# Optimization experiments

Hardware: AMD Instinct MI355X
Metric: run time of the kernel (lower is better)

The kernel has to match this reference:

```python
import jax, jax.numpy as jnp
import numpy as np

N = 100_000      # nodes
E = 1_600_000    # directed edges (before self-loops)
F_IN = 256       # input node features
H = 128          # hidden_dim
HEADS = 2
C_HEAD = H // HEADS  # 64, GATConv out_channels per head
G = 128          # graphs in batch
NCLS = 10
NEG_SLOPE = 0.2  # PyG GATConv default


def setup_inputs() -> dict:
    key = jax.random.key(0)
    ks = jax.random.split(key, 20)
    p = lambda k, shape: (jax.random.normal(k, shape, jnp.float32) * 0.05)
    x = jax.random.normal(ks[0], (N, F_IN), jnp.float32)
    edge_index = jax.random.randint(ks[1], (2, E), 0, N, dtype=jnp.int64)
    batch = jnp.sort(jax.random.randint(ks[2], (N,), 0, G, dtype=jnp.int64))
    return dict(
        x=x, edge_index=edge_index, batch=batch,
        pre_w=p(ks[3], (F_IN, H)), pre_b=p(ks[4], (H,)),
        w1=p(ks[5], (H, H)), asrc1=p(ks[6], (HEADS, C_HEAD)), adst1=p(ks[7], (HEADS, C_HEAD)), b1=p(ks[8], (H,)),
        w2=p(ks[9], (H, H)), asrc2=p(ks[10], (HEADS, C_HEAD)), adst2=p(ks[11], (HEADS, C_HEAD)), b2=p(ks[12], (H,)),
        post_w1=p(ks[13], (H, H)), post_b1=p(ks[14], (H,)),
        post_w2=p(ks[15], (H, NCLS)), post_b2=p(ks[16], (NCLS,)),
    )


def _gat_conv(h_in, w, a_src, a_dst, b, src, dst):
    # h: [N, heads, c]
    h = (h_in @ w).reshape(N, HEADS, C_HEAD)
    alpha_src = jnp.sum(h * a_src, axis=-1)  # [N, heads]
    alpha_dst = jnp.sum(h * a_dst, axis=-1)  # [N, heads]
    e = jax.nn.leaky_relu(alpha_src[src] + alpha_dst[dst], NEG_SLOPE)  # [E+N, heads]
    # numerically stable softmax over incoming edges of each destination node
    m = jax.ops.segment_max(e, dst, num_segments=N)
    ex = jnp.exp(e - m[dst])
    denom = jax.ops.segment_sum(ex, dst, num_segments=N)
    alpha = ex / denom[dst]                                           # [E+N, heads]
    out = jax.ops.segment_sum(h[src] * alpha[:, :, None], dst, num_segments=N)
    return out.reshape(N, H) + b  # concat heads + bias


def reference(x, edge_index, batch, pre_w, pre_b,
              w1, asrc1, adst1, b1, w2, asrc2, adst2, b2,
              post_w1, post_b1, post_w2, post_b2):
    # PyG GATConv default add_self_loops=True
    loop = jnp.arange(N, dtype=edge_index.dtype)
    src = jnp.concatenate([edge_index[0], loop])
    dst = jnp.concatenate([edge_index[1], loop])

    h = jax.nn.relu(x @ pre_w + pre_b)
    reprs = jax.ops.segment_sum(h, batch, num_segments=G)
    h = jax.nn.relu(_gat_conv(h, w1, asrc1, adst1, b1, src, dst))
    reprs = reprs + jax.ops.segment_sum(h, batch, num_segments=G)
    h = jax.nn.relu(_gat_conv(h, w2, asrc2, adst2, b2, src, dst))
    reprs = reprs + jax.ops.segment_sum(h, batch, num_segments=G)
    z = jax.nn.relu(reprs @ post_w1 + post_b1) @ post_w2 + post_b2
    return jax.nn.log_softmax(z, axis=-1)
```

## Files before the change

### kernel.cpp

```cpp
#include <hip/hip_runtime.h>
#include <hip/hip_bf16.h>
#include <math.h>

#define NNODES 100000
#define NEDGES 1600000
#define FIN 256
#define HDIM 128
#define NGRAPH 128
#define NCLS 10
#define NEG 0.2f

#define NBUCK 98
#define EPB 4096
#define EBLK ((NEDGES + EPB - 1) / EPB)

typedef short bf8 __attribute__((ext_vector_type(8)));
typedef float f4 __attribute__((ext_vector_type(4)));

__device__ __forceinline__ float lrelu(float x) { return x > 0.f ? x : NEG * x; }

__device__ __forceinline__ unsigned short f2bf(float f) {
  union { float f; unsigned int u; } v; v.f = f;
  unsigned int r = v.u + 0x7fffu + ((v.u >> 16) & 1u);
  return (unsigned short)(r >> 16);
}
__device__ __forceinline__ float bf2f(unsigned short u) {
  union { unsigned int u; float f; } v; v.u = ((unsigned int)u) << 16; return v.f;
}
__device__ __forceinline__ float fast_rcp(float x) {
  float r;
  asm("v_rcp_f32 %0, %1" : "=v"(r) : "v"(x));
  return r;
}
__device__ __forceinline__ unsigned cvt_pk_bf16(float lo, float hi) {
  unsigned r;
  asm("v_cvt_pk_bf16_f32 %0, %1, %2" : "=v"(r) : "v"(lo), "v"(hi));
  return r;
}
__device__ __forceinline__ unsigned short pk_fp8(float a, float b) {
  return (unsigned short)__builtin_amdgcn_cvt_pk_fp8_f32(a, b, 0, false);
}
__device__ __forceinline__ float fp8_lo(unsigned p) {
  return __builtin_amdgcn_cvt_f32_fp8(p, 0);
}
__device__ __forceinline__ float fp8_hi(unsigned p) {
  return __builtin_amdgcn_cvt_f32_fp8(p, 1);
}

__global__ __launch_bounds__(256) void convert_transpose(const float* __restrict__ w,
                                                         unsigned short* __restrict__ wt,
                                                         int K) {
  int i = blockIdx.x * 256 + threadIdx.x;
  if (i >= K * 128) return;
  int k = i >> 7, n = i & 127;
  wt[n * K + k] = f2bf(w[(size_t)k * 128 + n]);
}

__global__ __launch_bounds__(256) void gemm_mfma(const void* __restrict__ Av,
                                                 int a_bf16,
                                                 const unsigned short* __restrict__ Bt,
                                                 const float* __restrict__ bias,
                                                 unsigned short* __restrict__ Cb,
                                                 unsigned short* __restrict__ Cp,
                                                 const float* __restrict__ a_src,
                                                 const float* __restrict__ a_dst,
                                                 float* __restrict__ o_as,
                                                 float* __restrict__ o_ad,
                                                 int M, int K, int dorelu) {
  __shared__ bf8 As[256];
  __shared__ bf8 Bs[512];
  int tid = threadIdx.x;
  int wv = tid >> 6, lane = tid & 63;
  int quad = lane >> 4, m16 = lane & 15;
  int row0 = blockIdx.x * 64;

  int l0 = tid & 63;
  int rA = row0 + (tid >> 6) * 16 + (l0 & 15); if (rA > M - 1) rA = M - 1;
  int nB0 = (tid >> 6) * 16 + (l0 & 15);
  int nB1 = (4 + (tid >> 6)) * 16 + (l0 & 15);
  int cOff = (l0 >> 4) * 8;

  float4 f0a, f0b, f1a, f1b;
  bf8 h0, h1, b00, b01, b10, b11;

  auto loadT0 = [&](int kb) {
    if (a_bf16) {
      h0 = *reinterpret_cast<const bf8*>((const unsigned short*)Av + (size_t)rA * K + kb + cOff);
    } else {
      const float* p = (const float*)Av + (size_t)rA * K + kb + cOff;
      f0a = *reinterpret_cast<const float4*>(p);
      f0b = *reinterpret_cast<const float4*>(p + 4);
    }
    b00 = *reinterpret_cast<const bf8*>(&Bt[(size_t)nB0 * K + kb + cOff]);
    b01 = *reinterpret_cast<const bf8*>(&Bt[(size_t)nB1 * K + kb + cOff]);
  };
  auto loadT1 = [&](int kb) {
    if (a_bf16) {
      h1 = *reinterpret_cast<const bf8*>((const unsigned short*)Av + (size_t)rA * K + kb + cOff);
    } else {
      const float* p = (const float*)Av + (size_t)rA * K + kb + cOff;
      f1a = *reinterpret_cast<const float4*>(p);
      f1b = *reinterpret_cast<const float4*>(p + 4);
    }
    b10 = *reinterpret_cast<const bf8*>(&Bt[(size_t)nB0 * K + kb + cOff]);
    b11 = *reinterpret_cast<const bf8*>(&Bt[(size_t)nB1 * K + kb + cOff]);
  };
  auto cvt8 = [&](float4 a, float4 b) -> bf8 {
    bf8 v;
    v[0] = (short)f2bf(a.x); v[1] = (short)f2bf(a.y);
    v[2] = (short)f2bf(a.z); v[3] = (short)f2bf(a.w);
    v[4] = (short)f2bf(b.x); v[5] = (short)f2bf(b.y);
    v[6] = (short)f2bf(b.z); v[7] = (short)f2bf(b.w);
    return v;
  };

  f4 acc[8];
#pragma unroll
  for (int b = 0; b < 8; ++b) acc[b] = (f4){0.f, 0.f, 0.f, 0.f};

  loadT0(0);
  loadT1(32);
  for (int kb = 0; kb < K; kb += 64) {
    __syncthreads();
    As[tid] = a_bf16 ? h0 : cvt8(f0a, f0b);
    Bs[tid] = b00; Bs[tid + 256] = b01;
    __syncthreads();
    if (kb + 64 < K) loadT0(kb + 64);
    {
      bf8 af = As[wv * 64 + lane];
#pragma unroll
      for (int tn = 0; tn < 8; ++tn) {
        bf8 bfm = Bs[tn * 64 + lane];
        acc[tn] = __builtin_amdgcn_mfma_f32_16x16x32_bf16(af, bfm, acc[tn], 0, 0, 0);
      }
    }
    __syncthreads();
    As[tid] = a_bf16 ? h1 : cvt8(f1a, f1b);
    Bs[tid] = b10; Bs[tid + 256] = b11;
    __syncthreads();
    if (kb + 96 < K) loadT1(kb + 96);
    {
      bf8 af = As[wv * 64 + lane];
#pragma unroll
      for (int tn = 0; tn < 8; ++tn) {
        bf8 bfm = Bs[tn * 64 + lane];
        acc[tn] = __builtin_amdgcn_mfma_f32_16x16x32_bf16(af, bfm, acc[tn], 0, 0, 0);
      }
    }
  }

  if (Cp) {
    if (a_src) {
      float aS[8], aD[8];
#pragma unroll
      for (int tn = 0; tn < 4; ++tn) {
        aS[tn]     = a_src[tn * 16 + m16];
        aS[tn + 4] = a_src[64 + tn * 16 + m16];
        aD[tn]     = a_dst[tn * 16 + m16];
        aD[tn + 4] = a_dst[64 + tn * 16 + m16];
      }
#pragma unroll
      for (int r = 0; r < 4; ++r) {
        int row = row0 + wv * 16 + quad * 4 + r;
        float ps0 = 0.f, ps1 = 0.f, pd0 = 0.f, pd1 = 0.f;
#pragma unroll
        for (int tn = 0; tn < 4; ++tn) {
          float v0 = acc[tn][r], v1 = acc[tn + 4][r];
          ps0 = fmaf(v0, aS[tn], ps0);
          ps1 = fmaf(v1, aS[tn + 4], ps1);
          pd0 = fmaf(v0, aD[tn], pd0);
          pd1 = fmaf(v1, aD[tn + 4], pd1);
        }
#pragma unroll
        for (int o = 8; o; o >>= 1) {
          ps0 += __shfl_xor(ps0, o); ps1 += __shfl_xor(ps1, o);
          pd0 += __shfl_xor(pd0, o); pd1 += __shfl_xor(pd1, o);
        }
        if (m16 == 0 && row < M) {
          o_as[2 * row] = ps0; o_as[2 * row + 1] = ps1;
          o_ad[2 * row] = pd0; o_ad[2 * row + 1] = pd1;
        }
      }
    }
#pragma unroll
    for (int tn = 0; tn < 4; ++tn)
#pragma unroll
      for (int r = 0; r < 4; ++r) {
        int row = row0 + wv * 16 + quad * 4 + r;
        if (row < M) {
          Cp[(size_t)row * 64 + tn * 16 + m16] = pk_fp8(acc[tn][r], acc[tn + 4][r]);
        }
      }
  } else {
#pragma unroll
    for (int tn = 0; tn < 8; ++tn) {
      float bv = bias ? bias[tn * 16 + m16] : 0.f;
#pragma unroll
      for (int r = 0; r < 4; ++r) {
        int row = row0 + wv * 16 + quad * 4 + r;
        if (row < M) {
          float v = acc[tn][r] + bv;
          if (dorelu) v = fmaxf(v, 0.f);
          Cb[(size_t)row * 128 + tn * 16 + m16] = f2bf(v);
        }
      }
    }
  }
}

__global__ void find_starts(const int* __restrict__ batch, int* __restrict__ gstart) {
  int g = threadIdx.x;
  if (g > NGRAPH) return;
  if (g == NGRAPH) { gstart[g] = NNODES; return; }
  int lo = 0, hi = NNODES;
  while (lo < hi) { int mid = (lo + hi) >> 1; if (batch[mid] < g) lo = mid + 1; else hi = mid; }
  gstart[g] = lo;
}

__global__ __launch_bounds__(256) void bin_count(const int* __restrict__ edst,
                                                 int* __restrict__ blockHist) {
  __shared__ int hist[NBUCK];
  int t = threadIdx.x, blk = blockIdx.x;
  if (t < NBUCK) hist[t] = 0;
  __syncthreads();
  int e0 = blk * EPB;
#pragma unroll
  for (int it = 0; it < EPB / 256; ++it) {
    int e = e0 + it * 256 + t;
    if (e < NEDGES) atomicAdd(&hist[((unsigned)edst[e]) >> 10], 1);
  }
  __syncthreads();
  if (t < NBUCK) blockHist[blk * NBUCK + t] = hist[t];
}

__global__ __launch_bounds__(512) void colscan(const int* __restrict__ blockHist,
                                               int* __restrict__ blockBaseCol,
                                               int* __restrict__ bucket_total) {
  __shared__ int s[512];
  int b = blockIdx.x, t = threadIdx.x;
  int v = (t < EBLK) ? blockHist[t * NBUCK + b] : 0;
  s[t] = v;
  __syncthreads();
  for (int off = 1; off < 512; off <<= 1) {
    int u = (t >= off) ? s[t - off] : 0;
    __syncthreads();
    s[t] += u;
    __syncthreads();
  }
  if (t < EBLK) blockBaseCol[b * EBLK + t] = s[t] - v;
  if (t == 511) bucket_total[b] = s[511];
}

__global__ __launch_bounds__(128) void bscan(const int* __restrict__ bucket_total,
                                             int* __restrict__ bucket_ptr) {
  __shared__ int s[128];
  int t = threadIdx.x;
  int v = (t < NBUCK) ? bucket_total[t] : 0;
  s[t] = v;
  __syncthreads();
  for (int off = 1; off < 128; off <<= 1) {
    int u = (t >= off) ? s[t - off] : 0;
    __syncthreads();
    s[t] += u;
    __syncthreads();
  }
  if (t < NBUCK) bucket_ptr[t] = s[t] - v;
  if (t == 127) bucket_ptr[NBUCK] = s[127];
}

__global__ __launch_bounds__(512) void bin_place(const int* __restrict__ esrc,
                                                 const int* __restrict__ edst,
                                                 const int* __restrict__ blockBaseCol,
                                                 const int* __restrict__ bucket_ptr,
                                                 unsigned* __restrict__ stagingG) {
  __shared__ int hist[NBUCK + 1], lbase[NBUCK + 1], lcur[NBUCK + 1], cbase[NBUCK];
  __shared__ int tmp[128];
  __shared__ uint2 st[EPB];
  int t = threadIdx.x, blk = blockIdx.x;
  if (t < NBUCK + 1) hist[t] = 0;
  __syncthreads();
  int e0 = blk * EPB;
#pragma unroll
  for (int it = 0; it < EPB / 512; ++it) {
    int e = e0 + it * 512 + t;
    int b = NBUCK;
    if (e < NEDGES) b = ((unsigned)edst[e]) >> 10;
    atomicAdd(&hist[b], 1);
  }
  __syncthreads();
  if (t < 128) tmp[t] = (t < NBUCK + 1) ? hist[t] : 0;
  __syncthreads();
  for (int off = 1; off < 128; off <<= 1) {
    int u = 0;
    if (t < 128 && t >= off) u = tmp[t - off];
    __syncthreads();
    if (t < 128) tmp[t] += u;
    __syncthreads();
  }
  if (t < NBUCK + 1) { int ex = tmp[t] - hist[t]; lbase[t] = ex; lcur[t] = ex; }
  if (t < NBUCK) cbase[t] = bucket_ptr[t] + blockBaseCol[t * EBLK + blk];
  __syncthreads();
#pragma unroll
  for (int it = 0; it < EPB / 512; ++it) {
    int e = e0 + it * 512 + t;
    unsigned s = 0, d = 0xFFFFFFFFu;
    if (e < NEDGES) { s = (unsigned)esrc[e]; d = (unsigned)edst[e]; }
    int b = (d == 0xFFFFFFFFu) ? NBUCK : (int)(d >> 10);
    int slot = atomicAdd(&lcur[b], 1);
    st[slot] = make_uint2(s, d);
  }
  __syncthreads();
  for (int i = t; i < EPB; i += 512) {
    uint2 ed = st[i];
    if (ed.y == 0xFFFFFFFFu) continue;
    int b = (int)(ed.y >> 10);
    stagingG[cbase[b] + (i - lbase[b])] = ((ed.y & 1023u) << 17) | ed.x;
  }
}

__global__ __launch_bounds__(1024) void bucket_csr_fused(const unsigned* __restrict__ stagingG,
                                                         const int* __restrict__ bucket_ptr,
                                                         int* __restrict__ row_ptr,
                                                         int* __restrict__ colv) {
  __shared__ int dl[1024];
  __shared__ int cur[1024];
  int b = blockIdx.x, t = threadIdx.x;
  dl[t] = 0;
  __syncthreads();
  int s0 = bucket_ptr[b], s1 = bucket_ptr[b + 1];
  for (int j = s0 + t; j < s1; j += 1024)
    atomicAdd(&dl[stagingG[j] >> 17], 1);
  __syncthreads();
  int myDeg = dl[t];
  for (int off = 1; off < 1024; off <<= 1) {
    int u = (t >= off) ? dl[t - off] : 0;
    __syncthreads();
    dl[t] += u;
    __syncthreads();
  }
  int rp = s0 + dl[t] - myDeg;
  cur[t] = rp;
  int n = (b << 10) + t;
  if (n < NNODES) row_ptr[n] = rp;
  if (n == NNODES - 1) row_ptr[NNODES] = rp + myDeg;
  __syncthreads();
  for (int j = s0 + t; j < s1; j += 1024) {
    unsigned v = stagingG[j];
    int pos = atomicAdd(&cur[v >> 17], 1);
    colv[pos] = (int)(v & 0x1FFFFu);
  }
}

__global__ __launch_bounds__(256) void aggregate(const unsigned short* __restrict__ hwb,
                                                 const float* __restrict__ a_s,
                                                 const float* __restrict__ a_d,
                                                 const int* __restrict__ row_ptr,
                                                 const int* __restrict__ colv,
                                                 const float* __restrict__ bias,
                                                 unsigned short* __restrict__ out) {
  int i = (blockIdx.x * 256 + threadIdx.x) >> 6;
  int lane = threadIdx.x & 63;
  if (i >= NNODES) return;
  i = __builtin_amdgcn_readfirstlane(i);

  float ad0 = a_d[2 * i], ad1 = a_d[2 * i + 1];
  int start = row_ptr[i], end = row_ptr[i + 1];
  int deg = end - start;
  float ws0 = __expf(lrelu(a_s[2 * i] + ad0));
  float ws1 = __expf(lrelu(a_s[2 * i + 1] + ad1));

  int sl = 0; float w0l = 0.f, w1l = 0.f;
  if (lane < deg) {
    sl = colv[start + lane];
    float2 av = *reinterpret_cast<const float2*>(&a_s[2 * sl]);
    w0l = __expf(lrelu(av.x + ad0));
    w1l = __expf(lrelu(av.y + ad1));
  }
  float d0 = w0l, d1 = w1l;
  for (int o = 32; o; o >>= 1) { d0 += __shfl_xor(d0, o); d1 += __shfl_xor(d1, o); }
  float den0 = d0 + ws0, den1 = d1 + ws1;

  unsigned ps = hwb[(size_t)i * 64 + lane];
  float acc0 = ws0 * fp8_lo(ps), acc1 = ws1 * fp8_hi(ps);

  int dmin = deg < 64 ? deg : 64;
  int t = 0;
  for (; t + 4 <= dmin; t += 4) {
    int s0 = __builtin_amdgcn_readlane(sl, t);
    int s1 = __builtin_amdgcn_readlane(sl, t + 1);
    int s2 = __builtin_amdgcn_readlane(sl, t + 2);
    int s3 = __builtin_amdgcn_readlane(sl, t + 3);
    unsigned q0 = hwb[(size_t)s0 * 64 + lane];
    unsigned q1 = hwb[(size_t)s1 * 64 + lane];
    unsigned q2 = hwb[(size_t)s2 * 64 + lane];
    unsigned q3 = hwb[(size_t)s3 * 64 + lane];
    float u0 = __uint_as_float(__builtin_amdgcn_readlane(__float_as_uint(w0l), t));
    float v0 = __uint_as_float(__builtin_amdgcn_readlane(__float_as_uint(w1l), t));
    float u1 = __uint_as_float(__builtin_amdgcn_readlane(__float_as_uint(w0l), t + 1));
    float v1 = __uint_as_float(__builtin_amdgcn_readlane(__float_as_uint(w1l), t + 1));
    float u2 = __uint_as_float(__builtin_amdgcn_readlane(__float_as_uint(w0l), t + 2));
    float v2 = __uint_as_float(__builtin_amdgcn_readlane(__float_as_uint(w1l), t + 2));
    float u3 = __uint_as_float(__builtin_amdgcn_readlane(__float_as_uint(w0l), t + 3));
    float v3 = __uint_as_float(__builtin_amdgcn_readlane(__float_as_uint(w1l), t + 3));
    acc0 = fmaf(u0, fp8_lo(q0), acc0); acc1 = fmaf(v0, fp8_hi(q0), acc1);
    acc0 = fmaf(u1, fp8_lo(q1), acc0); acc1 = fmaf(v1, fp8_hi(q1), acc1);
    acc0 = fmaf(u2, fp8_lo(q2), acc0); acc1 = fmaf(v2, fp8_hi(q2), acc1);
    acc0 = fmaf(u3, fp8_lo(q3), acc0); acc1 = fmaf(v3, fp8_hi(q3), acc1);
  }
  for (; t < dmin; ++t) {
    int s = __builtin_amdgcn_readlane(sl, t);
    float u = __uint_as_float(__builtin_amdgcn_readlane(__float_as_uint(w0l), t));
    float v = __uint_as_float(__builtin_amdgcn_readlane(__float_as_uint(w1l), t));
    unsigned q = hwb[(size_t)s * 64 + lane];
    acc0 = fmaf(u, fp8_lo(q), acc0);
    acc1 = fmaf(v, fp8_hi(q), acc1);
  }
  for (int j = start + 64; j < end; ++j) {
    int s = colv[j];
    float2 av = *reinterpret_cast<const float2*>(&a_s[2 * s]);
    float w0 = __expf(lrelu(av.x + ad0));
    float w1 = __expf(lrelu(av.y + ad1));
    den0 += w0; den1 += w1;
    unsigned q = hwb[(size_t)s * 64 + lane];
    acc0 = fmaf(w0, fp8_lo(q), acc0);
    acc1 = fmaf(w1, fp8_hi(q), acc1);
  }

  float r0 = fast_rcp(den0), r1 = fast_rcp(den1);
  float o0 = fmaxf(acc0 * r0 + bias[lane], 0.f);
  float o1 = fmaxf(acc1 * r1 + bias[64 + lane], 0.f);
  unsigned pk = cvt_pk_bf16(o0, o1);
  out[(size_t)i * 128 + lane]      = (unsigned short)pk;
  out[(size_t)i * 128 + 64 + lane] = (unsigned short)(pk >> 16);
}

#define SEG_CHUNK 128
__global__ __launch_bounds__(128) void seg_sum_fast(const unsigned short* __restrict__ h,
                                                    const int* __restrict__ batch,
                                                    const int* __restrict__ gstart,
                                                    float* __restrict__ reprs) {
  int n0 = blockIdx.x * SEG_CHUNK;
  if (n0 >= NNODES) return;
  int nend = n0 + SEG_CHUNK; if (nend > NNODES) nend = NNODES;
  int tid = threadIdx.x;
  int r = n0;
  while (r < nend) {
    int g = batch[r];
    int segend = gstart[g + 1]; if (segend > nend) segend = nend;
    float a0 = 0.f, a1 = 0.f, a2 = 0.f, a3 = 0.f;
    for (; r + 3 < segend; r += 4) {
      a0 += bf2f(h[(size_t)r * 128 + tid]);
      a1 += bf2f(h[(size_t)(r + 1) * 128 + tid]);
      a2 += bf2f(h[(size_t)(r + 2) * 128 + tid]);
      a3 += bf2f(h[(size_t)(r + 3) * 128 + tid]);
    }
    for (; r < segend; ++r) a0 += bf2f(h[(size_t)r * 128 + tid]);
    atomicAdd(&reprs[g * 128 + tid], (a0 + a1) + (a2 + a3));
  }
}

__global__ __launch_bounds__(128) void head_kernel(const float* __restrict__ reprs,
                                                   const float* __restrict__ pw1,
                                                   const float* __restrict__ pb1,
                                                   const float* __restrict__ pw2,
                                                   const float* __restrict__ pb2,
                                                   float* __restrict__ out) {
  __shared__ float r[128], t1[128], z[NCLS];
  int g = blockIdx.x, tid = threadIdx.x;
  r[tid] = reprs[g * 128 + tid];
  __syncthreads();
  float acc = pb1[tid];
  for (int k = 0; k < 128; ++k) acc = fmaf(r[k], pw1[k * 128 + tid], acc);
  t1[tid] = fmaxf(acc, 0.f);
  __syncthreads();
  if (tid < NCLS) {
    float zz = pb2[tid];
    for (int k = 0; k < 128; ++k) zz = fmaf(t1[k], pw2[k * NCLS + tid], zz);
    z[tid] = zz;
  }
  __syncthreads();
  if (tid == 0) {
    float mx = -1e30f;
    for (int c = 0; c < NCLS; ++c) mx = fmaxf(mx, z[c]);
    float s = 0.f;
    for (int c = 0; c < NCLS; ++c) s += expf(z[c] - mx);
    float ls = logf(s) + mx;
    for (int c = 0; c < NCLS; ++c) out[g * NCLS + c] = z[c] - ls;
  }
}

extern "C" void kernel_launch(void* const* d_in, const int* in_sizes, int n_in,
                              void* d_out, int out_size, void* d_ws, size_t ws_size,
                              hipStream_t stream) {
  const float* x     = (const float*)d_in[0];
  const int*   eidx  = (const int*)d_in[1];
  const int*   batch = (const int*)d_in[2];
  const float* pre_w = (const float*)d_in[3];
  const float* pre_b = (const float*)d_in[4];
  const float* w1    = (const float*)d_in[5];
  const float* asrc1 = (const float*)d_in[6];
  const float* adst1 = (const float*)d_in[7];
  const float* b1    = (const float*)d_in[8];
  const float* w2    = (const float*)d_in[9];
  const float* asrc2 = (const float*)d_in[10];
  const float* adst2 = (const float*)d_in[11];
  const float* b2    = (const float*)d_in[12];
  const float* pw1   = (const float*)d_in[13];
  const float* pb1   = (const float*)d_in[14];
  const float* pw2   = (const float*)d_in[15];
  const float* pb2   = (const float*)d_in[16];
  float* out = (float*)d_out;

  const int* esrc = eidx;
  const int* edst = eidx + NEDGES;

  char* wsp = (char*)d_ws;
  size_t off = 0;
  auto alloc = [&](size_t bytes) -> void* {
    void* p = wsp + off;
    off += (bytes + 255) & ~(size_t)255;
    return p;
  };
  unsigned short* hb  = (unsigned short*)alloc((size_t)NNODES * 128 * 2);
  unsigned short* hwb = (unsigned short*)alloc((size_t)NNODES * 64 * 2);
  float* a_s         = (float*)alloc((size_t)NNODES * 2 * 4);
  float* a_d         = (float*)alloc((size_t)NNODES * 2 * 4);
  float* reprs       = (float*)alloc((size_t)NGRAPH * 128 * 4);
  int* gstart        = (int*)alloc((NGRAPH + 1) * 4);
  int* row_ptr       = (int*)alloc(((size_t)NNODES + 1) * 4);
  int* colv          = (int*)alloc((size_t)NEDGES * 4);
  unsigned short* wt_pre = (unsigned short*)alloc((size_t)128 * FIN * 2);
  unsigned short* wt1    = (unsigned short*)alloc((size_t)128 * HDIM * 2);
  unsigned short* wt2    = (unsigned short*)alloc((size_t)128 * HDIM * 2);
  int* blockHist     = (int*)alloc((size_t)EBLK * NBUCK * 4);
  int* blockBaseCol  = (int*)alloc((size_t)NBUCK * EBLK * 4);
  int* bucket_total  = (int*)alloc(NBUCK * 4);
  int* bucket_ptr    = (int*)alloc((NBUCK + 1) * 4);
  unsigned* stagingG = (unsigned*)alloc((size_t)NEDGES * 4);

  int wb = NNODES / 4;
  int sb = (NNODES + SEG_CHUNK - 1) / SEG_CHUNK;
  int gb = (NNODES + 63) / 64;

  convert_transpose<<<(FIN * 128 + 255) / 256, 256, 0, stream>>>(pre_w, wt_pre, FIN);
  convert_transpose<<<(HDIM * 128 + 255) / 256, 256, 0, stream>>>(w1, wt1, HDIM);
  convert_transpose<<<(HDIM * 128 + 255) / 256, 256, 0, stream>>>(w2, wt2, HDIM);

  hipMemsetAsync(reprs, 0, (size_t)NGRAPH * 128 * 4, stream);
  find_starts<<<1, 256, 0, stream>>>(batch, gstart);

  bin_count<<<EBLK, 256, 0, stream>>>(edst, blockHist);
  colscan<<<NBUCK, 512, 0, stream>>>(blockHist, blockBaseCol, bucket_total);
  bscan<<<1, 128, 0, stream>>>(bucket_total, bucket_ptr);
  bin_place<<<EBLK, 512, 0, stream>>>(esrc, edst, blockBaseCol, bucket_ptr, stagingG);
  bucket_csr_fused<<<NBUCK, 1024, 0, stream>>>(stagingG, bucket_ptr, row_ptr, colv);

  gemm_mfma<<<gb, 256, 0, stream>>>(x, 0, wt_pre, pre_b, hb, nullptr,
                                    nullptr, nullptr, nullptr, nullptr, NNODES, FIN, 1);
  seg_sum_fast<<<sb, 128, 0, stream>>>(hb, batch, gstart, reprs);

  gemm_mfma<<<gb, 256, 0, stream>>>(hb, 1, wt1, nullptr, nullptr, hwb,
                                    asrc1, adst1, a_s, a_d, NNODES, HDIM, 0);
  aggregate<<<wb, 256, 0, stream>>>(hwb, a_s, a_d, row_ptr, colv, b1, hb);
  seg_sum_fast<<<sb, 128, 0, stream>>>(hb, batch, gstart, reprs);

  gemm_mfma<<<gb, 256, 0, stream>>>(hb, 1, wt2, nullptr, nullptr, hwb,
                                    asrc2, adst2, a_s, a_d, NNODES, HDIM, 0);
  aggregate<<<wb, 256, 0, stream>>>(hwb, a_s, a_d, row_ptr, colv, b2, hb);
  seg_sum_fast<<<sb, 128, 0, stream>>>(hb, batch, gstart, reprs);

  head_kernel<<<NGRAPH, 128, 0, stream>>>(reprs, pw1, pb1, pw2, pb2, out);
}
```

Baseline: 473.8 us.

## Double GEMM row tile to 128 and stage edge weights in LDS for gather

```diff
diff --git a/kernel.cpp b/kernel.cpp
--- a/kernel.cpp
+++ b/kernel.cpp
@@ -16,6 +16,7 @@
 
 typedef short bf8 __attribute__((ext_vector_type(8)));
 typedef float f4 __attribute__((ext_vector_type(4)));
+typedef float f2v __attribute__((ext_vector_type(2)));
 
 __device__ __forceinline__ float lrelu(float x) { return x > 0.f ? x : NEG * x; }
 
@@ -40,11 +41,15 @@
 __device__ __forceinline__ unsigned short pk_fp8(float a, float b) {
   return (unsigned short)__builtin_amdgcn_cvt_pk_fp8_f32(a, b, 0, false);
 }
-__device__ __forceinline__ float fp8_lo(unsigned p) {
-  return __builtin_amdgcn_cvt_f32_fp8(p, 0);
-}
-__device__ __forceinline__ float fp8_hi(unsigned p) {
-  return __builtin_amdgcn_cvt_f32_fp8(p, 1);
+__device__ __forceinline__ f2v pk_unpack_fp8(unsigned p) {
+#if __has_builtin(__builtin_amdgcn_cvt_pk_f32_fp8)
+  return __builtin_amdgcn_cvt_pk_f32_fp8((int)p, false);
+#else
+  f2v r;
+  r.x = __builtin_amdgcn_cvt_f32_fp8(p, 0);
+  r.y = __builtin_amdgcn_cvt_f32_fp8(p, 1);
+  return r;
+#endif
 }
 
 __global__ __launch_bounds__(256) void convert_transpose(const float* __restrict__ w,
@@ -67,40 +72,48 @@
                                                  float* __restrict__ o_as,
                                                  float* __restrict__ o_ad,
                                                  int M, int K, int dorelu) {
-  __shared__ bf8 As[256];
+  __shared__ bf8 As[512];
   __shared__ bf8 Bs[512];
   int tid = threadIdx.x;
   int wv = tid >> 6, lane = tid & 63;
   int quad = lane >> 4, m16 = lane & 15;
-  int row0 = blockIdx.x * 64;
-
-  int l0 = tid & 63;
-  int rA = row0 + (tid >> 6) * 16 + (l0 & 15); if (rA > M - 1) rA = M - 1;
-  int nB0 = (tid >> 6) * 16 + (l0 & 15);
-  int nB1 = (4 + (tid >> 6)) * 16 + (l0 & 15);
-  int cOff = (l0 >> 4) * 8;
-
-  float4 f0a, f0b, f1a, f1b;
-  bf8 h0, h1, b00, b01, b10, b11;
+  int row0 = blockIdx.x * 128;
+
+  int rA0 = row0 + (tid >> 6) * 16 + (lane & 15); if (rA0 > M - 1) rA0 = M - 1;
+  int rA1 = rA0 + 64; if (rA1 > M - 1) rA1 = M - 1;
+  int nB0 = (tid >> 6) * 16 + (lane & 15);
+  int nB1 = (4 + (tid >> 6)) * 16 + (lane & 15);
+  int cOff = (lane >> 4) * 8;
+
+  float4 f0a, f0b, f0c, f0d, f1a, f1b, f1c, f1d;
+  bf8 h0a, h0b, h1a, h1b, b00, b01, b10, b11;
 
   auto loadT0 = [&](int kb) {
     if (a_bf16) {
-      h0 = *reinterpret_cast<const bf8*>((const unsigned short*)Av + (size_t)rA * K + kb + cOff);
+      h0a = *reinterpret_cast<const bf8*>((const unsigned short*)Av + (size_t)rA0 * K + kb + cOff);
+      h0b = *reinterpret_cast<const bf8*>((const unsigned short*)Av + (size_t)rA1 * K + kb + cOff);
     } else {
-      const float* p = (const float*)Av + (size_t)rA * K + kb + cOff;
-      f0a = *reinterpret_cast<const float4*>(p);
-      f0b = *reinterpret_cast<const float4*>(p + 4);
+      const float* p0 = (const float*)Av + (size_t)rA0 * K + kb + cOff;
+      const float* p1 = (const float*)Av + (size_t)rA1 * K + kb + cOff;
+      f0a = *reinterpret_cast<const float4*>(p0);
+      f0b = *reinterpret_cast<const float4*>(p0 + 4);
+      f0c = *reinterpret_cast<const float4*>(p1);
+      f0d = *reinterpret_cast<const float4*>(p1 + 4);
     }
     b00 = *reinterpret_cast<const bf8*>(&Bt[(size_t)nB0 * K + kb + cOff]);
     b01 = *reinterpret_cast<const bf8*>(&Bt[(size_t)nB1 * K + kb + cOff]);
   };
   auto loadT1 = [&](int kb) {
     if (a_bf16) {
-      h1 = *reinterpret_cast<const bf8*>((const unsigned short*)Av + (size_t)rA * K + kb + cOff);
+      h1a = *reinterpret_cast<const bf8*>((const unsigned short*)Av + (size_t)rA0 * K + kb + cOff);
+      h1b = *reinterpret_cast<const bf8*>((const unsigned short*)Av + (size_t)rA1 * K + kb + cOff);
     } else {
-      const float* p = (const float*)Av + (size_t)rA * K + kb + cOff;
-      f1a = *reinterpret_cast<const float4*>(p);
-      f1b = *reinterpret_cast<const float4*>(p + 4);
+      const float* p0 = (const float*)Av + (size_t)rA0 * K + kb + cOff;
+      const float* p1 = (const float*)Av + (size_t)rA1 * K + kb + cOff;
+      f1a = *reinterpret_cast<const float4*>(p0);
+      f1b = *reinterpret_cast<const float4*>(p0 + 4);
+      f1c = *reinterpret_cast<const float4*>(p1);
+      f1d = *reinterpret_cast<const float4*>(p1 + 4);
     }
     b10 = *reinterpret_cast<const bf8*>(&Bt[(size_t)nB0 * K + kb + cOff]);
     b11 = *reinterpret_cast<const bf8*>(&Bt[(size_t)nB1 * K + kb + cOff]);
@@ -114,37 +127,43 @@
     return v;
   };
 
-  f4 acc[8];
-#pragma unroll
-  for (int b = 0; b < 8; ++b) acc[b] = (f4){0.f, 0.f, 0.f, 0.f};
+  f4 acc[16];
+#pragma unroll
+  for (int b = 0; b < 16; ++b) acc[b] = (f4){0.f, 0.f, 0.f, 0.f};
 
   loadT0(0);
   loadT1(32);
   for (int kb = 0; kb < K; kb += 64) {
     __syncthreads();
-    As[tid] = a_bf16 ? h0 : cvt8(f0a, f0b);
+    As[tid]       = a_bf16 ? h0a : cvt8(f0a, f0b);
+    As[256 + tid] = a_bf16 ? h0b : cvt8(f0c, f0d);
     Bs[tid] = b00; Bs[tid + 256] = b01;
     __syncthreads();
     if (kb + 64 < K) loadT0(kb + 64);
     {
-      bf8 af = As[wv * 64 + lane];
+      bf8 af0 = As[wv * 64 + lane];
+      bf8 af1 = As[(wv + 4) * 64 + lane];
 #pragma unroll
       for (int tn = 0; tn < 8; ++tn) {
         bf8 bfm = Bs[tn * 64 + lane];
-        acc[tn] = __builtin_amdgcn_mfma_f32_16x16x32_bf16(af, bfm, acc[tn], 0, 0, 0);
+        acc[tn]     = __builtin_amdgcn_mfma_f32_16x16x32_bf16(af0, bfm, acc[tn], 0, 0, 0);
+        acc[8 + tn] = __builtin_amdgcn_mfma_f32_16x16x32_bf16(af1, bfm, acc[8 + tn], 0, 0, 0);
       }
     }
     __syncthreads();
-    As[tid] = a_bf16 ? h1 : cvt8(f1a, f1b);
+    As[tid]       = a_bf16 ? h1a : cvt8(f1a, f1b);
+    As[256 + tid] = a_bf16 ? h1b : cvt8(f1c, f1d);
     Bs[tid] = b10; Bs[tid + 256] = b11;
     __syncthreads();
     if (kb + 96 < K) loadT1(kb + 96);
     {
-      bf8 af = As[wv * 64 + lane];
+      bf8 af0 = As[wv * 64 + lane];
+      bf8 af1 = As[(wv + 4) * 64 + lane];
 #pragma unroll
       for (int tn = 0; tn < 8; ++tn) {
         bf8 bfm = Bs[tn * 64 + lane];
-        acc[tn] = __builtin_amdgcn_mfma_f32_16x16x32_bf16(af, bfm, acc[tn], 0, 0, 0);
+        acc[tn]     = __builtin_amdgcn_mfma_f32_16x16x32_bf16(af0, bfm, acc[tn], 0, 0, 0);
+        acc[8 + tn] = __builtin_amdgcn_mfma_f32_16x16x32_bf16(af1, bfm, acc[8 + tn], 0, 0, 0);
       }
     }
   }
@@ -160,51 +179,59 @@
         aD[tn + 4] = a_dst[64 + tn * 16 + m16];
       }
 #pragma unroll
-      for (int r = 0; r < 4; ++r) {
-        int row = row0 + wv * 16 + quad * 4 + r;
-        float ps0 = 0.f, ps1 = 0.f, pd0 = 0.f, pd1 = 0.f;
-#pragma unroll
-        for (int tn = 0; tn < 4; ++tn) {
-          float v0 = acc[tn][r], v1 = acc[tn + 4][r];
-          ps0 = fmaf(v0, aS[tn], ps0);
-          ps1 = fmaf(v1, aS[tn + 4], ps1);
-          pd0 = fmaf(v0, aD[tn], pd0);
-          pd1 = fmaf(v1, aD[tn + 4], pd1);
-        }
-#pragma unroll
-        for (int o = 8; o; o >>= 1) {
-          ps0 += __shfl_xor(ps0, o); ps1 += __shfl_xor(ps1, o);
-          pd0 += __shfl_xor(pd0, o); pd1 += __shfl_xor(pd1, o);
-        }
-        if (m16 == 0 && row < M) {
-          o_as[2 * row] = ps0; o_as[2 * row + 1] = ps1;
-          o_ad[2 * row] = pd0; o_ad[2 * row + 1] = pd1;
+      for (int mt = 0; mt < 2; ++mt) {
+#pragma unroll
+        for (int r = 0; r < 4; ++r) {
+          int row = row0 + mt * 64 + wv * 16 + quad * 4 + r;
+          float ps0 = 0.f, ps1 = 0.f, pd0 = 0.f, pd1 = 0.f;
+#pragma unroll
+          for (int tn = 0; tn < 4; ++tn) {
+            float v0 = acc[mt * 8 + tn][r], v1 = acc[mt * 8 + tn + 4][r];
+            ps0 = fmaf(v0, aS[tn], ps0);
+            ps1 = fmaf(v1, aS[tn + 4], ps1);
+            pd0 = fmaf(v0, aD[tn], pd0);
+            pd1 = fmaf(v1, aD[tn + 4], pd1);
+          }
+#pragma unroll
+          for (int o = 8; o; o >>= 1) {
+            ps0 += __shfl_xor(ps0, o); ps1 += __shfl_xor(ps1, o);
+            pd0 += __shfl_xor(pd0, o); pd1 += __shfl_xor(pd1, o);
+          }
+          if (m16 == 0 && row < M) {
+            o_as[2 * row] = ps0; o_as[2 * row + 1] = ps1;
+            o_ad[2 * row] = pd0; o_ad[2 * row + 1] = pd1;
+          }
         }
       }
     }
 #pragma unroll
-    for (int tn = 0; tn < 4; ++tn)
-#pragma unroll
-      for (int r = 0; r < 4; ++r) {
-        int row = row0 + wv * 16 + quad * 4 + r;
-        if (row < M) {
-          Cp[(size_t)row * 64 + tn * 16 + m16] = pk_fp8(acc[tn][r], acc[tn + 4][r]);
+    for (int mt = 0; mt < 2; ++mt)
+#pragma unroll
+      for (int tn = 0; tn < 4; ++tn)
+#pragma unroll
+        for (int r = 0; r < 4; ++r) {
+          int row = row0 + mt * 64 + wv * 16 + quad * 4 + r;
+          if (row < M) {
+            Cp[(size_t)row * 64 + tn * 16 + m16] =
+                pk_fp8(acc[mt * 8 + tn][r], acc[mt * 8 + tn + 4][r]);
+          }
+        }
+  } else {
+#pragma unroll
+    for (int mt = 0; mt < 2; ++mt)
+#pragma unroll
+      for (int tn = 0; tn < 8; ++tn) {
+        float bv = bias ? bias[tn * 16 + m16] : 0.f;
+#pragma unroll
+        for (int r = 0; r < 4; ++r) {
+          int row = row0 + mt * 64 + wv * 16 + quad * 4 + r;
+          if (row < M) {
+            float v = acc[mt * 8 + tn][r] + bv;
+            if (dorelu) v = fmaxf(v, 0.f);
+            Cb[(size_t)row * 128 + tn * 16 + m16] = f2bf(v);
+          }
         }
       }
-  } else {
-#pragma unroll
-    for (int tn = 0; tn < 8; ++tn) {
-      float bv = bias ? bias[tn * 16 + m16] : 0.f;
-#pragma unroll
-      for (int r = 0; r < 4; ++r) {
-        int row = row0 + wv * 16 + quad * 4 + r;
-        if (row < M) {
-          float v = acc[tn][r] + bv;
-          if (dorelu) v = fmaxf(v, 0.f);
-          Cb[(size_t)row * 128 + tn * 16 + m16] = f2bf(v);
-        }
-      }
-    }
   }
 }
 
@@ -358,10 +385,12 @@
                                                  const int* __restrict__ colv,
                                                  const float* __restrict__ bias,
                                                  unsigned short* __restrict__ out) {
+  __shared__ float2 wsh[256];
   int i = (blockIdx.x * 256 + threadIdx.x) >> 6;
   int lane = threadIdx.x & 63;
   if (i >= NNODES) return;
   i = __builtin_amdgcn_readfirstlane(i);
+  int wbase = (threadIdx.x >> 6) * 64;
 
   float ad0 = a_d[2 * i], ad1 = a_d[2 * i + 1];
   int start = row_ptr[i], end = row_ptr[i + 1];
@@ -376,45 +405,33 @@
     w0l = __expf(lrelu(av.x + ad0));
     w1l = __expf(lrelu(av.y + ad1));
   }
+  wsh[wbase + lane] = make_float2(w0l, w1l);
   float d0 = w0l, d1 = w1l;
   for (int o = 32; o; o >>= 1) { d0 += __shfl_xor(d0, o); d1 += __shfl_xor(d1, o); }
   float den0 = d0 + ws0, den1 = d1 + ws1;
 
   unsigned ps = hwb[(size_t)i * 64 + lane];
-  float acc0 = ws0 * fp8_lo(ps), acc1 = ws1 * fp8_hi(ps);
+  f2v pv = pk_unpack_fp8(ps);
+  float acc0 = ws0 * pv.x, acc1 = ws1 * pv.y;
 
   int dmin = deg < 64 ? deg : 64;
   int t = 0;
-  for (; t + 4 <= dmin; t += 4) {
-    int s0 = __builtin_amdgcn_readlane(sl, t);
-    int s1 = __builtin_amdgcn_readlane(sl, t + 1);
-    int s2 = __builtin_amdgcn_readlane(sl, t + 2);
-    int s3 = __builtin_amdgcn_readlane(sl, t + 3);
-    unsigned q0 = hwb[(size_t)s0 * 64 + lane];
-    unsigned q1 = hwb[(size_t)s1 * 64 + lane];
-    unsigned q2 = hwb[(size_t)s2 * 64 + lane];
-    unsigned q3 = hwb[(size_t)s3 * 64 + lane];
-    float u0 = __uint_as_float(__builtin_amdgcn_readlane(__float_as_uint(w0l), t));
-    float v0 = __uint_as_float(__builtin_amdgcn_readlane(__float_as_uint(w1l), t));
-    float u1 = __uint_as_float(__builtin_amdgcn_readlane(__float_as_uint(w0l), t + 1));
-    float v1 = __uint_as_float(__builtin_amdgcn_readlane(__float_as_uint(w1l), t + 1));
-    float u2 = __uint_as_float(__builtin_amdgcn_readlane(__float_as_uint(w0l), t + 2));
-    float v2 = __uint_as_float(__builtin_amdgcn_readlane(__float_as_uint(w1l), t + 2));
-    float u3 = __uint_as_float(__builtin_amdgcn_readlane(__float_as_uint(w0l), t + 3));
-    float v3 = __uint_as_float(__builtin_amdgcn_readlane(__float_as_uint(w1l), t + 3));
-    acc0 = fmaf(u0, fp8_lo(q0), acc0); acc1 = fmaf(v0, fp8_hi(q0), acc1);
-    acc0 = fmaf(u1, fp8_lo(q1), acc0); acc1 = fmaf(v1, fp8_hi(q1), acc1);
-    acc0 = fmaf(u2, fp8_lo(q2), acc0); acc1 = fmaf(v2, fp8_hi(q2), acc1);
-    acc0 = fmaf(u3, fp8_lo(q3), acc0); acc1 = fmaf(v3, fp8_hi(q3), acc1);
-  }
-  for (; t < dmin; ++t) {
-    int s = __builtin_amdgcn_readlane(sl, t);
-    float u = __uint_as_float(__builtin_amdgcn_readlane(__float_as_uint(w0l), t));
-    float v = __uint_as_float(__builtin_amdgcn_readlane(__float_as_uint(w1l), t));
-    unsigned q = hwb[(size_t)s * 64 + lane];
-    acc0 = fmaf(u, fp8_lo(q), acc0);
-    acc1 = fmaf(v, fp8_hi(q), acc1);
-  }
+#define GSTEP(T)                                                               \
+  {                                                                            \
+    int s = __builtin_amdgcn_readlane(sl, (T));                                \
+    unsigned q = hwb[(size_t)s * 64 + lane];                                   \
+    float2 w = wsh[wbase + (T)];                    \
+    f2v xv = pk_unpack_fp8(q);                                                 \
+    acc0 = fmaf(w.x, xv.x, acc0);                                              \
+    acc1 = fmaf(w.y, xv.y, acc1);                                              \
+  }
+  for (; t + 8 <= dmin; t += 8) {
+    GSTEP(t);     GSTEP(t + 1); GSTEP(t + 2); GSTEP(t + 3);
+    GSTEP(t + 4); GSTEP(t + 5); GSTEP(t + 6); GSTEP(t + 7);
+  }
+  for (; t < dmin; ++t) { GSTEP(t); }
+#undef GSTEP
+
   for (int j = start + 64; j < end; ++j) {
     int s = colv[j];
     float2 av = *reinterpret_cast<const float2*>(&a_s[2 * s]);
@@ -422,8 +439,9 @@
     float w1 = __expf(lrelu(av.y + ad1));
     den0 += w0; den1 += w1;
     unsigned q = hwb[(size_t)s * 64 + lane];
-    acc0 = fmaf(w0, fp8_lo(q), acc0);
-    acc1 = fmaf(w1, fp8_hi(q), acc1);
+    f2v xv = pk_unpack_fp8(q);
+    acc0 = fmaf(w0, xv.x, acc0);
+    acc1 = fmaf(w1, xv.y, acc1);
   }
 
   float r0 = fast_rcp(den0), r1 = fast_rcp(den1);
@@ -540,7 +558,7 @@
 
   int wb = NNODES / 4;
   int sb = (NNODES + SEG_CHUNK - 1) / SEG_CHUNK;
-  int gb = (NNODES + 63) / 64;
+  int gb = (NNODES + 127) / 128;
 
   convert_transpose<<<(FIN * 128 + 255) / 256, 256, 0, stream>>>(pre_w, wt_pre, FIN);
   convert_transpose<<<(HDIM * 128 + 255) / 256, 256, 0, stream>>>(w1, wt1, HDIM);
```

Result: no change. 474.8 us (+0.2%).
